# Optimization experiments

Measured on AMD Instinct MI355X. Metric: run time of the kernel, lower is better.

The kernel has to match this reference:

```python
import jax, jax.numpy as jnp
import numpy as np

SPATIAL = ((100, 100), (50, 50), (25, 25), (13, 13))
STARTS = [0]
for _h, _w in SPATIAL[:-1]:
    STARTS.append(STARTS[-1] + _h * _w)
L_TOTAL = sum(h * w for h, w in SPATIAL)  # 13294
D, DFFN, NL, NH, NP = 256, 1024, 4, 8, 4
DH = D // NH
EPS = 1e-5


def _ln(x, g, b):
    mu = x.mean(-1, keepdims=True)
    var = ((x - mu) ** 2).mean(-1, keepdims=True)
    return (x - mu) * jax.lax.rsqrt(var + EPS) * g + b


def _bilinear(v_l, x, y, H, W):
    # v_l: [B,NH,H*W,DH]; x,y: [B,NH,Q*NP] pixel coords (grid_sample align_corners=False, zero padding)
    x0f = jnp.floor(x); y0f = jnp.floor(y)
    lx, ly = x - x0f, y - y0f
    x0 = x0f.astype(jnp.int32); y0 = y0f.astype(jnp.int32)
    acc = 0.0
    for dx, dy, w in ((0, 0, (1 - lx) * (1 - ly)), (1, 0, lx * (1 - ly)),
                      (0, 1, (1 - lx) * ly), (1, 1, lx * ly)):
        xi, yi = x0 + dx, y0 + dy
        valid = (xi >= 0) & (xi < W) & (yi >= 0) & (yi < H)
        idx = jnp.clip(yi, 0, H - 1) * W + jnp.clip(xi, 0, W - 1)
        g = jnp.take_along_axis(v_l, idx[..., None], axis=2)  # [B,NH,Q*NP,DH]
        acc = acc + g * (w * valid.astype(w.dtype))[..., None]
    return acc


def _msdeform(query, value_in, ref, norm_wh, Woff, boff, Wattn, battn, Wval, bval, Wout, bout):
    B, Q, _ = query.shape
    v = (value_in @ Wval + bval).reshape(B, L_TOTAL, NH, DH)
    off = (query @ Woff + boff).reshape(B, Q, NH, NL, NP, 2)
    aw = (query @ Wattn + battn).reshape(B, Q, NH, NL * NP)
    aw = jax.nn.softmax(aw, axis=-1).reshape(B, Q, NH, NL, NP)
    # normalized sampling locations in [0,1]: ref + offset / (W,H)
    loc = ref[:, :, None, :, None, :] + off / norm_wh[None, None, None, :, None, :]
    out = 0.0
    for l, (H, W) in enumerate(SPATIAL):
        s = STARTS[l]
        v_l = v[:, s:s + H * W].transpose(0, 2, 1, 3)          # [B,NH,HW,DH]
        loc_l = loc[:, :, :, l].transpose(0, 2, 1, 3, 4)       # [B,NH,Q,NP,2]
        x = (loc_l[..., 0] * W - 0.5).reshape(B, NH, Q * NP)
        y = (loc_l[..., 1] * H - 0.5).reshape(B, NH, Q * NP)
        samp = _bilinear(v_l, x, y, H, W).reshape(B, NH, Q, NP, DH)
        w_l = aw[:, :, :, l].transpose(0, 2, 1, 3)             # [B,NH,Q,NP]
        out = out + (samp * w_l[..., None]).sum(3)             # [B,NH,Q,DH]
    out = out.transpose(0, 2, 1, 3).reshape(B, Q, D)
    return out @ Wout + bout


def setup_inputs() -> dict:
    key = jax.random.key(0)
    ks = jax.random.split(key, 12)
    B = 4
    s = 0.02
    return {
        "src": jax.random.normal(ks[0], (B, L_TOTAL, D), jnp.float32),
        "pos": jax.random.normal(ks[1], (B, L_TOTAL, D), jnp.float32),
        "reference_points": jax.random.uniform(ks[2], (B, L_TOTAL, NL, 2), jnp.float32),
        "spatial_shapes": jnp.array(SPATIAL, jnp.int32),
        "level_start_index": jnp.array(STARTS, jnp.int32),
        "W_off": jax.random.normal(ks[3], (D, NH * NL * NP * 2), jnp.float32) * 0.01,
        "b_off": jax.random.normal(ks[4], (NH * NL * NP * 2,), jnp.float32) * 0.5,
        "W_attn": jax.random.normal(ks[5], (D, NH * NL * NP), jnp.float32) * s,
        "b_attn": jnp.zeros((NH * NL * NP,), jnp.float32),
        "W_val": jax.random.normal(ks[6], (D, D), jnp.float32) * s,
        "b_val": jnp.zeros((D,), jnp.float32),
        "W_out": jax.random.normal(ks[7], (D, D), jnp.float32) * s,
        "b_out": jnp.zeros((D,), jnp.float32),
        "ln_sa_g": jnp.ones((D,), jnp.float32),
        "ln_sa_b": jnp.zeros((D,), jnp.float32),
        "W1": jax.random.normal(ks[8], (D, DFFN), jnp.float32) * s,
        "b1": jnp.zeros((DFFN,), jnp.float32),
        "W2": jax.random.normal(ks[9], (DFFN, D), jnp.float32) * s,
        "b2": jnp.zeros((D,), jnp.float32),
        "ln_ff_g": jnp.ones((D,), jnp.float32),
        "ln_ff_b": jnp.zeros((D,), jnp.float32),
    }


def reference(src, pos, reference_points, spatial_shapes, level_start_index,
              W_off, b_off, W_attn, b_attn, W_val, b_val, W_out, b_out,
              ln_sa_g, ln_sa_b, W1, b1, W2, b2, ln_ff_g, ln_ff_b):
    # offset normalizer is (W, H) per level
    norm_wh = jnp.stack([spatial_shapes[:, 1], spatial_shapes[:, 0]], -1).astype(src.dtype)
    q = src + pos  # with_pos_embed
    sa = _msdeform(q, src, reference_points, norm_wh,
                   W_off, b_off, W_attn, b_attn, W_val, b_val, W_out, b_out)
    x = _ln(sa + src, ln_sa_g, ln_sa_b)          # dropout = identity (eval)
    y = jnp.maximum(x @ W1 + b1, 0.0) @ W2 + b2  # relu FFN
    return _ln(y + x, ln_ff_g, ln_ff_b)
```

## Files before the change

### kernel.cpp

```cpp
#include <hip/hip_runtime.h>
#include <hip/hip_bf16.h>

typedef __hip_bfloat16 bf16;
typedef short bf16x8 __attribute__((ext_vector_type(8)));
typedef float f32x4  __attribute__((ext_vector_type(4)));

#define ROWS 53176
#define LTOT 13294

__device__ __forceinline__ float b2f(bf16 v) { return __bfloat162float(v); }

__device__ __forceinline__ void gl2lds16(const void* g, void* l) {
    __builtin_amdgcn_global_load_lds(
        (const __attribute__((address_space(1))) unsigned*)g,
        (__attribute__((address_space(3))) unsigned*)l, 16, 0, 0);
}

template<bool RELU>
__global__ __launch_bounds__(256)
void mfma_gemm_n(const bf16* __restrict__ A, const bf16* __restrict__ Bt,
                 const float* __restrict__ bias, bf16* __restrict__ C,
                 int M, int N, int K)
{
    __shared__ __align__(16) short As[128 * 32];
    __shared__ __align__(16) short Bs[128 * 32];
    const int tid  = threadIdx.x;
    const int wave = tid >> 6, lane = tid & 63;
    const int m0 = blockIdx.y * 128, n0 = blockIdx.x * 128;
    const int lrow = lane >> 2, lcol = lane & 3;
    const int quad = lane >> 4;

    f32x4 acc[4][4];
#pragma unroll
    for (int i = 0; i < 4; ++i)
#pragma unroll
        for (int j = 0; j < 4; ++j) acc[i][j] = (f32x4){0.f, 0.f, 0.f, 0.f};

    const int wM = (wave >> 1) * 64, wN = (wave & 1) * 64;
    const int foff = (lane & 15) * 32 + quad * 8;

    for (int kk = 0; kk < K; kk += 32) {
#pragma unroll
        for (int q = 0; q < 2; ++q) {
            int rbase = wave * 32 + q * 16;
            int row = rbase + lrow;
            gl2lds16(A  + (size_t)(m0 + row) * K + kk + lcol * 8, &As[rbase * 32]);
            gl2lds16(Bt + (size_t)(n0 + row) * K + kk + lcol * 8, &Bs[rbase * 32]);
        }
        __syncthreads();
        bf16x8 af[4], bfr[4];
#pragma unroll
        for (int i = 0; i < 4; ++i)
            af[i] = *(const bf16x8*)&As[(wM + i * 16) * 32 + foff];
#pragma unroll
        for (int j = 0; j < 4; ++j)
            bfr[j] = *(const bf16x8*)&Bs[(wN + j * 16) * 32 + foff];
#pragma unroll
        for (int i = 0; i < 4; ++i)
#pragma unroll
            for (int j = 0; j < 4; ++j)
                acc[i][j] = __builtin_amdgcn_mfma_f32_16x16x32_bf16(bfr[j], af[i], acc[i][j], 0, 0, 0);
        __syncthreads();
    }

    float4 b4[4];
#pragma unroll
    for (int j = 0; j < 4; ++j)
        b4[j] = *(const float4*)&bias[n0 + wN + j * 16 + quad * 4];

#pragma unroll
    for (int i = 0; i < 4; ++i) {
        int gm = m0 + wM + i * 16 + (lane & 15);
        if (gm >= M) continue;
#pragma unroll
        for (int j = 0; j < 4; ++j) {
            int gn = n0 + wN + j * 16 + quad * 4;
            union { bf16 h[4]; uint2 u2; } pk;
#pragma unroll
            for (int r = 0; r < 4; ++r) {
                float v = acc[i][j][r] + ((const float*)&b4[j])[r];
                if (RELU) v = fmaxf(v, 0.f);
                pk.h[r] = __float2bfloat16(v);
            }
            *(uint2*)&C[(size_t)gm * N + gn] = pk.u2;
        }
    }
}

template<typename OT>
__global__ __launch_bounds__(512)
void mfma_gemm_ln(const bf16* __restrict__ A, const bf16* __restrict__ Bt,
                  const float* __restrict__ bias, const bf16* __restrict__ res,
                  OT* __restrict__ C, const float* __restrict__ gam,
                  const float* __restrict__ bet, int M, int K)
{
    __shared__ __align__(16) short As[128 * 32];
    __shared__ __align__(16) short Bs[256 * 32];
    __shared__ float rsum[128], rsq[128];
    const int tid  = threadIdx.x;
    const int wave = tid >> 6, lane = tid & 63;
    const int m0 = blockIdx.x * 128;
    const int lrow = lane >> 2, lcol = lane & 3;
    const int quad = lane >> 4;
    if (tid < 128) { rsum[tid] = 0.f; rsq[tid] = 0.f; }

    f32x4 acc[4][4];
#pragma unroll
    for (int i = 0; i < 4; ++i)
#pragma unroll
        for (int j = 0; j < 4; ++j) acc[i][j] = (f32x4){0.f, 0.f, 0.f, 0.f};

    const int wM = (wave >> 2) * 64, wN = (wave & 3) * 64;
    const int foff = (lane & 15) * 32 + quad * 8;

    for (int kk = 0; kk < K; kk += 32) {
#pragma unroll
        for (int q = 0; q < 3; ++q) {
            int r = wave * 48 + q * 16;
            if (r < 128) {
                gl2lds16(A + (size_t)(m0 + r + lrow) * K + kk + lcol * 8, &As[r * 32]);
            } else {
                int rr = r - 128;
                gl2lds16(Bt + (size_t)(rr + lrow) * K + kk + lcol * 8, &Bs[rr * 32]);
            }
        }
        __syncthreads();
        bf16x8 af[4], bfr[4];
#pragma unroll
        for (int i = 0; i < 4; ++i)
            af[i] = *(const bf16x8*)&As[(wM + i * 16) * 32 + foff];
#pragma unroll
        for (int j = 0; j < 4; ++j)
            bfr[j] = *(const bf16x8*)&Bs[(wN + j * 16) * 32 + foff];
#pragma unroll
        for (int i = 0; i < 4; ++i)
#pragma unroll
            for (int j = 0; j < 4; ++j)
                acc[i][j] = __builtin_amdgcn_mfma_f32_16x16x32_bf16(bfr[j], af[i], acc[i][j], 0, 0, 0);
        __syncthreads();
    }

    float4 b4[4], g4[4], be4[4];
#pragma unroll
    for (int j = 0; j < 4; ++j) {
        int gn = wN + j * 16 + quad * 4;
        b4[j]  = *(const float4*)&bias[gn];
        g4[j]  = *(const float4*)&gam[gn];
        be4[j] = *(const float4*)&bet[gn];
    }

    float lsum[4], lsq[4];
#pragma unroll
    for (int i = 0; i < 4; ++i) {
        int gm = m0 + wM + i * 16 + (lane & 15);
        lsum[i] = 0.f; lsq[i] = 0.f;
#pragma unroll
        for (int j = 0; j < 4; ++j) {
            int gn = wN + j * 16 + quad * 4;
            float r4[4] = {0.f, 0.f, 0.f, 0.f};
            if (gm < M) {
                uint2 ru = *(const uint2*)&res[(size_t)gm * 256 + gn];
                const bf16* rh = (const bf16*)&ru;
#pragma unroll
                for (int r = 0; r < 4; ++r) r4[r] = b2f(rh[r]);
            }
#pragma unroll
            for (int r = 0; r < 4; ++r) {
                float v = acc[i][j][r] + ((const float*)&b4[j])[r] + r4[r];
                acc[i][j][r] = v;
                lsum[i] += v;
                lsq[i]  += v * v;
            }
        }
#pragma unroll
        for (int mask = 16; mask <= 32; mask <<= 1) {
            lsum[i] += __shfl_xor(lsum[i], mask);
            lsq[i]  += __shfl_xor(lsq[i], mask);
        }
    }
    if (quad == 0) {
#pragma unroll
        for (int i = 0; i < 4; ++i) {
            atomicAdd(&rsum[wM + i * 16 + (lane & 15)], lsum[i]);
            atomicAdd(&rsq [wM + i * 16 + (lane & 15)], lsq[i]);
        }
    }
    __syncthreads();

#pragma unroll
    for (int i = 0; i < 4; ++i) {
        int lr = wM + i * 16 + (lane & 15);
        int gm = m0 + lr;
        if (gm >= M) continue;
        float mean = rsum[lr] * (1.f / 256.f);
        float var  = rsq[lr] * (1.f / 256.f) - mean * mean;
        float rstd = rsqrtf(fmaxf(var, 0.f) + 1e-5f);
#pragma unroll
        for (int j = 0; j < 4; ++j) {
            int gn = wN + j * 16 + quad * 4;
            if constexpr (sizeof(OT) == 2) {
                union { bf16 h[4]; uint2 u2; } pk;
#pragma unroll
                for (int r = 0; r < 4; ++r)
                    pk.h[r] = __float2bfloat16((acc[i][j][r] - mean) * rstd *
                              ((const float*)&g4[j])[r] + ((const float*)&be4[j])[r]);
                *(uint2*)&((bf16*)C)[(size_t)gm * 256 + gn] = pk.u2;
            } else {
                float4 o;
#pragma unroll
                for (int r = 0; r < 4; ++r)
                    ((float*)&o)[r] = (acc[i][j][r] - mean) * rstd *
                              ((const float*)&g4[j])[r] + ((const float*)&be4[j])[r];
                *(float4*)&((float*)C)[(size_t)gm * 256 + gn] = o;
            }
        }
    }
}

__global__ void cast_qs_kernel(const float* __restrict__ s, const float* __restrict__ p,
                               bf16* __restrict__ sb, bf16* __restrict__ qb, int n4)
{
    int i = blockIdx.x * 256 + threadIdx.x;
    if (i >= n4) return;
    float4 sv = ((const float4*)s)[i];
    float4 pv = ((const float4*)p)[i];
    union { bf16 h[4]; uint2 u; } a, b;
    a.h[0] = __float2bfloat16(sv.x); a.h[1] = __float2bfloat16(sv.y);
    a.h[2] = __float2bfloat16(sv.z); a.h[3] = __float2bfloat16(sv.w);
    b.h[0] = __float2bfloat16(sv.x + pv.x); b.h[1] = __float2bfloat16(sv.y + pv.y);
    b.h[2] = __float2bfloat16(sv.z + pv.z); b.h[3] = __float2bfloat16(sv.w + pv.w);
    ((uint2*)sb)[i] = a.u;
    ((uint2*)qb)[i] = b.u;
}

__global__ void wcast_all(const float* __restrict__ Wval, const float* __restrict__ Woff,
                          const float* __restrict__ Wattn, const float* __restrict__ Wout,
                          const float* __restrict__ W1, const float* __restrict__ W2,
                          const float* __restrict__ boff, const float* __restrict__ battn,
                          bf16* __restrict__ Wval_t, bf16* __restrict__ Wcat_t,
                          bf16* __restrict__ Wout_t, bf16* __restrict__ W1_t,
                          bf16* __restrict__ W2_t, float* __restrict__ bcat)
{
    int e = blockIdx.x * 256 + threadIdx.x;
    if (e < 384) bcat[e] = (e < 256) ? boff[e] : battn[e - 256];
    if (e < 65536) {
        int n = e >> 8, k = e & 255;
        Wval_t[e] = __float2bfloat16(Wval[k * 256 + n]);
    } else if (e < 163840) {
        int i = e - 65536; int n = i >> 8, k = i & 255;
        float w = (n < 256) ? Woff[k * 256 + n] : Wattn[k * 128 + (n - 256)];
        Wcat_t[i] = __float2bfloat16(w);
    } else if (e < 229376) {
        int i = e - 163840; int n = i >> 8, k = i & 255;
        Wout_t[i] = __float2bfloat16(Wout[k * 256 + n]);
    } else if (e < 491520) {
        int i = e - 229376; int n = i >> 8, k = i & 255;
        W1_t[i] = __float2bfloat16(W1[k * 1024 + n]);
    } else if (e < 753664) {
        int i = e - 491520; int n = i >> 10, k = i & 1023;
        W2_t[i] = __float2bfloat16(W2[k * 256 + n]);
    }
}

__global__ __launch_bounds__(256)
void sample_kernel(const bf16* __restrict__ v, const bf16* __restrict__ ocat,
                   const float* __restrict__ ref, bf16* __restrict__ samp)
{
    __shared__ int4 tab[16][33];
    const int tid = threadIdx.x;
    const int grp = tid >> 4, lane = tid & 15;
    const int gidx = blockIdx.x * 16 + grp;
    const int h = gidx & 7, bq = gidx >> 3, b = bq / LTOT;

    {
        const int p = lane, l = p >> 2, pp = p & 3;
        const int W = (l == 0) ? 100 : (l == 1) ? 50 : (l == 2) ? 25 : 13;
        const int S = (l == 0) ? 0 : (l == 1) ? 10000 : (l == 2) ? 12500 : 13125;
        const float fW = (float)W;
        float rx = ref[(size_t)bq * 8 + l * 2 + 0];
        float ry = ref[(size_t)bq * 8 + l * 2 + 1];
        const bf16* ob = ocat + (size_t)bq * 384;
        float ox = b2f(ob[h * 32 + l * 8 + pp * 2 + 0]);
        float oy = b2f(ob[h * 32 + l * 8 + pp * 2 + 1]);
        float lg = b2f(ob[256 + h * 16 + p]);
        float m = lg;
#pragma unroll
        for (int mask = 1; mask <= 8; mask <<= 1) m = fmaxf(m, __shfl_xor(m, mask));
        float ev = __expf(lg - m);
        float s = ev;
#pragma unroll
        for (int mask = 1; mask <= 8; mask <<= 1) s += __shfl_xor(s, mask);
        float wgt = ev / s;

        float x = fmaf(rx, fW, ox - 0.5f);
        float y = fmaf(ry, fW, oy - 0.5f);
        float x0f = floorf(x), y0f = floorf(y);
        float lx = x - x0f, ly = y - y0f;
        int x0 = (int)x0f, y0 = (int)y0f;
        float tw[4] = {(1.f - lx) * (1.f - ly), lx * (1.f - ly),
                       (1.f - lx) * ly,         lx * ly};
        const int base = (b * LTOT + S) * 512 + h * 64;
        int  o[4]; float w[4];
#pragma unroll
        for (int t = 0; t < 4; ++t) {
            int xi = x0 + (t & 1), yi = y0 + (t >> 1);
            bool ok = (xi >= 0) & (xi < W) & (yi >= 0) & (yi < W);
            o[t] = ok ? base + (yi * W + xi) * 512 : 0;
            w[t] = ok ? wgt * tw[t] : 0.f;
        }
        tab[grp][p * 2 + 0] = make_int4(o[0], __float_as_int(w[0]), o[1], __float_as_int(w[1]));
        tab[grp][p * 2 + 1] = make_int4(o[2], __float_as_int(w[2]), o[3], __float_as_int(w[3]));
    }
    __syncthreads();

    const int lofs = lane * 4;
    const char* vc = (const char*)v;
    float a0 = 0.f, a1 = 0.f;
#pragma unroll 4
    for (int e2 = 0; e2 < 32; ++e2) {
        int4 q = tab[grp][e2];
        unsigned u0 = *(const unsigned*)(vc + (size_t)(unsigned)(q.x + lofs));
        unsigned u1 = *(const unsigned*)(vc + (size_t)(unsigned)(q.z + lofs));
        float w0 = __int_as_float(q.y), w1 = __int_as_float(q.w);
        a0 += w0 * __uint_as_float(u0 << 16);
        a1 += w0 * __uint_as_float(u0);
        a0 += w1 * __uint_as_float(u1 << 16);
        a1 += w1 * __uint_as_float(u1);
    }
    union { struct { bf16 a, b; } h2; unsigned u; } r;
    r.h2.a = __float2bfloat16(a0);
    r.h2.b = __float2bfloat16(a1);
    *(unsigned*)((char*)samp + (size_t)gidx * 64 + lane * 4) = r.u;
}

extern "C" void kernel_launch(void* const* d_in, const int* in_sizes, int n_in,
                              void* d_out, int out_size, void* d_ws, size_t ws_size,
                              hipStream_t stream)
{
    const float* src     = (const float*)d_in[0];
    const float* pos     = (const float*)d_in[1];
    const float* ref     = (const float*)d_in[2];
    const float* W_off   = (const float*)d_in[5];
    const float* b_off   = (const float*)d_in[6];
    const float* W_attn  = (const float*)d_in[7];
    const float* b_attn  = (const float*)d_in[8];
    const float* W_val   = (const float*)d_in[9];
    const float* b_val   = (const float*)d_in[10];
    const float* W_out   = (const float*)d_in[11];
    const float* b_out   = (const float*)d_in[12];
    const float* ln_sa_g = (const float*)d_in[13];
    const float* ln_sa_b = (const float*)d_in[14];
    const float* W1      = (const float*)d_in[15];
    const float* b1      = (const float*)d_in[16];
    const float* W2      = (const float*)d_in[17];
    const float* b2      = (const float*)d_in[18];
    const float* ln_ff_g = (const float*)d_in[19];
    const float* ln_ff_b = (const float*)d_in[20];

    char* ws = (char*)d_ws;
    bf16* sb     = (bf16*)(ws);
    bf16* qb     = (bf16*)(ws + 27226112);
    bf16* samp   = (bf16*)(ws + 27226112);
    bf16* vbuf   = (bf16*)(ws + 54452224);
    bf16* ocat   = (bf16*)(ws + 81678336);
    bf16* xb16   = (bf16*)(ws + 122517504);
    bf16* hbuf   = (bf16*)(ws);
    bf16* Wval_t = (bf16*)(ws + 149743616);
    bf16* Wcat_t = (bf16*)(ws + 149874688);
    float* bcat  = (float*)(ws + 150071296);
    bf16* Wout_t = (bf16*)(ws + 150072832);
    bf16* W1_t   = (bf16*)(ws + 150203904);
    bf16* W2_t   = (bf16*)(ws + 150728192);
    float* outf  = (float*)d_out;

    dim3 blk(256);

    cast_qs_kernel<<<dim3((ROWS * 64 + 255) / 256), blk, 0, stream>>>(src, pos, sb, qb, ROWS * 64);
    wcast_all<<<dim3(2944), blk, 0, stream>>>(W_val, W_off, W_attn, W_out, W1, W2,
                                              b_off, b_attn,
                                              Wval_t, Wcat_t, Wout_t, W1_t, W2_t, bcat);

    mfma_gemm_n<false><<<dim3(2, 416), blk, 0, stream>>>(sb, Wval_t, b_val, vbuf, ROWS, 256, 256);
    mfma_gemm_n<false><<<dim3(3, 416), blk, 0, stream>>>(qb, Wcat_t, bcat, ocat, ROWS, 384, 256);
    sample_kernel<<<dim3(ROWS * 8 / 16), blk, 0, stream>>>(vbuf, ocat, ref, samp);
    mfma_gemm_ln<bf16><<<dim3(416), dim3(512), 0, stream>>>(
        samp, Wout_t, b_out, sb, xb16, ln_sa_g, ln_sa_b, ROWS, 256);
    mfma_gemm_n<true><<<dim3(8, 416), blk, 0, stream>>>(xb16, W1_t, b1, hbuf, ROWS, 1024, 256);
    mfma_gemm_ln<float><<<dim3(416), dim3(512), 0, stream>>>(
        hbuf, W2_t, b2, xb16, outf, ln_ff_g, ln_ff_b, ROWS, 1024);
}
```

Measured before the change: 504.4 us.

## Keep weight tiles resident in swizzled LDS and stream activations from global

The GEMM kernels are restructured so the whole weight slice for a block's N-tile (full K) is loaded once into a 64KB XOR-swizzled LDS buffer. Each wave then reads its A rows directly from global memory, with no per-K-step LDS staging or barriers. The LayerNorm GEMMs now compute 32 rows per wave across all 256 columns and do the row reduction in-wave with shuffles, which removes the LDS atomics and the extra barrier. The trade-offs are higher register pressure (32 accumulators per lane), A loads from global that are not coalesced through LDS, and the large LDS footprint limiting occupancy to two blocks per CU.

New measurement: 541.6 us. 7.4% more time.

```diff
diff --git a/kernel.cpp b/kernel.cpp
--- a/kernel.cpp
+++ b/kernel.cpp
@@ -17,64 +17,72 @@
 }
 
 template<bool RELU>
-__global__ __launch_bounds__(256)
-void mfma_gemm_n(const bf16* __restrict__ A, const bf16* __restrict__ Bt,
-                 const float* __restrict__ bias, bf16* __restrict__ C,
-                 int M, int N, int K)
-{
-    __shared__ __align__(16) short As[128 * 32];
-    __shared__ __align__(16) short Bs[128 * 32];
+__global__ __launch_bounds__(256, 2)
+void gemm_bs_n(const bf16* __restrict__ A, const bf16* __restrict__ Bt,
+               const float* __restrict__ bias, bf16* __restrict__ C,
+               int M, int N)
+{
+    __shared__ __align__(16) char Bsb[65536];
     const int tid  = threadIdx.x;
     const int wave = tid >> 6, lane = tid & 63;
-    const int m0 = blockIdx.y * 128, n0 = blockIdx.x * 128;
-    const int lrow = lane >> 2, lcol = lane & 3;
-    const int quad = lane >> 4;
-
-    f32x4 acc[4][4];
+    const int l15 = lane & 15, quad = lane >> 4;
+    const int swz = (lane & 7) << 4;
+    const int m0 = blockIdx.y * 256, n0 = blockIdx.x * 128;
+
+    const char* Btb = (const char*)(Bt + (size_t)n0 * 256);
+#pragma unroll
+    for (int it = 0; it < 16; ++it) {
+        int c = it * 256 + tid;
+        int srcoff = (c * 16) ^ (((c >> 5) & 7) << 4);
+        gl2lds16(Btb + srcoff, Bsb + (it * 256 + wave * 64) * 16);
+    }
+
+    const bf16* aptr[4];
+#pragma unroll
+    for (int i = 0; i < 4; ++i) {
+        int r = m0 + wave * 64 + i * 16 + l15;
+        if (r > M - 1) r = M - 1;
+        aptr[i] = A + (size_t)r * 256;
+    }
+
+    f32x4 acc[4][8];
 #pragma unroll
     for (int i = 0; i < 4; ++i)
 #pragma unroll
-        for (int j = 0; j < 4; ++j) acc[i][j] = (f32x4){0.f, 0.f, 0.f, 0.f};
-
-    const int wM = (wave >> 1) * 64, wN = (wave & 1) * 64;
-    const int foff = (lane & 15) * 32 + quad * 8;
-
-    for (int kk = 0; kk < K; kk += 32) {
-#pragma unroll
-        for (int q = 0; q < 2; ++q) {
-            int rbase = wave * 32 + q * 16;
-            int row = rbase + lrow;
-            gl2lds16(A  + (size_t)(m0 + row) * K + kk + lcol * 8, &As[rbase * 32]);
-            gl2lds16(Bt + (size_t)(n0 + row) * K + kk + lcol * 8, &Bs[rbase * 32]);
-        }
-        __syncthreads();
-        bf16x8 af[4], bfr[4];
+        for (int j = 0; j < 8; ++j) acc[i][j] = (f32x4){0.f, 0.f, 0.f, 0.f};
+
+    __syncthreads();
+
+#pragma unroll
+    for (int kc = 0; kc < 8; ++kc) {
+        bf16x8 af[4], bfr[8];
 #pragma unroll
         for (int i = 0; i < 4; ++i)
-            af[i] = *(const bf16x8*)&As[(wM + i * 16) * 32 + foff];
-#pragma unroll
-        for (int j = 0; j < 4; ++j)
-            bfr[j] = *(const bf16x8*)&Bs[(wN + j * 16) * 32 + foff];
+            af[i] = *(const bf16x8*)(aptr[i] + kc * 32 + quad * 8);
+#pragma unroll
+        for (int j = 0; j < 8; ++j) {
+            int boff = ((j * 16 + l15) * 512 + kc * 64 + quad * 16) ^ swz;
+            bfr[j] = *(const bf16x8*)&Bsb[boff];
+        }
 #pragma unroll
         for (int i = 0; i < 4; ++i)
 #pragma unroll
-            for (int j = 0; j < 4; ++j)
+            for (int j = 0; j < 8; ++j)
                 acc[i][j] = __builtin_amdgcn_mfma_f32_16x16x32_bf16(bfr[j], af[i], acc[i][j], 0, 0, 0);
-        __syncthreads();
-    }
-
-    float4 b4[4];
-#pragma unroll
-    for (int j = 0; j < 4; ++j)
-        b4[j] = *(const float4*)&bias[n0 + wN + j * 16 + quad * 4];
+    }
+
+    float4 b4[8];
+#pragma unroll
+    for (int j = 0; j < 8; ++j)
+        b4[j] = *(const float4*)&bias[n0 + j * 16 + quad * 4];
 
 #pragma unroll
     for (int i = 0; i < 4; ++i) {
-        int gm = m0 + wM + i * 16 + (lane & 15);
+        int gm = m0 + wave * 64 + i * 16 + l15;
         if (gm >= M) continue;
 #pragma unroll
-        for (int j = 0; j < 4; ++j) {
-            int gn = n0 + wN + j * 16 + quad * 4;
+        for (int j = 0; j < 8; ++j) {
+            int gn = n0 + j * 16 + quad * 4;
             union { bf16 h[4]; uint2 u2; } pk;
 #pragma unroll
             for (int r = 0; r < 4; ++r) {
@@ -87,78 +95,75 @@
     }
 }
 
-template<typename OT>
-__global__ __launch_bounds__(512)
-void mfma_gemm_ln(const bf16* __restrict__ A, const bf16* __restrict__ Bt,
-                  const float* __restrict__ bias, const bf16* __restrict__ res,
-                  OT* __restrict__ C, const float* __restrict__ gam,
-                  const float* __restrict__ bet, int M, int K)
-{
-    __shared__ __align__(16) short As[128 * 32];
-    __shared__ __align__(16) short Bs[256 * 32];
-    __shared__ float rsum[128], rsq[128];
+template<typename OT, int K>
+__global__ __launch_bounds__(256, 2)
+void gemm_bs_ln(const bf16* __restrict__ A, const bf16* __restrict__ Bt,
+                const float* __restrict__ bias, const bf16* __restrict__ res,
+                OT* __restrict__ C, const float* __restrict__ gam,
+                const float* __restrict__ bet, int M)
+{
+    __shared__ __align__(16) char Bsb[65536];
     const int tid  = threadIdx.x;
     const int wave = tid >> 6, lane = tid & 63;
+    const int l15 = lane & 15, quad = lane >> 4;
+    const int swz = (lane & 7) << 4;
     const int m0 = blockIdx.x * 128;
-    const int lrow = lane >> 2, lcol = lane & 3;
-    const int quad = lane >> 4;
-    if (tid < 128) { rsum[tid] = 0.f; rsq[tid] = 0.f; }
-
-    f32x4 acc[4][4];
-#pragma unroll
-    for (int i = 0; i < 4; ++i)
-#pragma unroll
-        for (int j = 0; j < 4; ++j) acc[i][j] = (f32x4){0.f, 0.f, 0.f, 0.f};
-
-    const int wM = (wave >> 2) * 64, wN = (wave & 3) * 64;
-    const int foff = (lane & 15) * 32 + quad * 8;
-
-    for (int kk = 0; kk < K; kk += 32) {
-#pragma unroll
-        for (int q = 0; q < 3; ++q) {
-            int r = wave * 48 + q * 16;
-            if (r < 128) {
-                gl2lds16(A + (size_t)(m0 + r + lrow) * K + kk + lcol * 8, &As[r * 32]);
-            } else {
-                int rr = r - 128;
-                gl2lds16(Bt + (size_t)(rr + lrow) * K + kk + lcol * 8, &Bs[rr * 32]);
-            }
+
+    const bf16* aptr[2];
+#pragma unroll
+    for (int i = 0; i < 2; ++i) {
+        int r = m0 + wave * 32 + i * 16 + l15;
+        if (r > M - 1) r = M - 1;
+        aptr[i] = A + (size_t)r * K;
+    }
+
+    f32x4 acc[2][16];
+#pragma unroll
+    for (int i = 0; i < 2; ++i)
+#pragma unroll
+        for (int j = 0; j < 16; ++j) acc[i][j] = (f32x4){0.f, 0.f, 0.f, 0.f};
+
+    for (int kc = 0; kc < K / 128; ++kc) {
+#pragma unroll
+        for (int it = 0; it < 16; ++it) {
+            int c = it * 256 + tid;
+            int row = c >> 4, col = c & 15;
+            size_t srcoff = (size_t)row * (K * 2) + kc * 256
+                          + ((col * 16) ^ ((row & 7) << 4));
+            gl2lds16((const char*)Bt + srcoff, Bsb + (it * 256 + wave * 64) * 16);
         }
         __syncthreads();
-        bf16x8 af[4], bfr[4];
-#pragma unroll
-        for (int i = 0; i < 4; ++i)
-            af[i] = *(const bf16x8*)&As[(wM + i * 16) * 32 + foff];
-#pragma unroll
-        for (int j = 0; j < 4; ++j)
-            bfr[j] = *(const bf16x8*)&Bs[(wN + j * 16) * 32 + foff];
-#pragma unroll
-        for (int i = 0; i < 4; ++i)
-#pragma unroll
-            for (int j = 0; j < 4; ++j)
-                acc[i][j] = __builtin_amdgcn_mfma_f32_16x16x32_bf16(bfr[j], af[i], acc[i][j], 0, 0, 0);
+#pragma unroll
+        for (int t = 0; t < 4; ++t) {
+            bf16x8 af[2], bfr[16];
+#pragma unroll
+            for (int i = 0; i < 2; ++i)
+                af[i] = *(const bf16x8*)(aptr[i] + kc * 128 + t * 32 + quad * 8);
+#pragma unroll
+            for (int j = 0; j < 16; ++j) {
+                int boff = ((j * 16 + l15) * 256 + t * 64 + quad * 16) ^ swz;
+                bfr[j] = *(const bf16x8*)&Bsb[boff];
+            }
+#pragma unroll
+            for (int i = 0; i < 2; ++i)
+#pragma unroll
+                for (int j = 0; j < 16; ++j)
+                    acc[i][j] = __builtin_amdgcn_mfma_f32_16x16x32_bf16(bfr[j], af[i], acc[i][j], 0, 0, 0);
+        }
         __syncthreads();
     }
 
-    float4 b4[4], g4[4], be4[4];
-#pragma unroll
-    for (int j = 0; j < 4; ++j) {
-        int gn = wN + j * 16 + quad * 4;
-        b4[j]  = *(const float4*)&bias[gn];
-        g4[j]  = *(const float4*)&gam[gn];
-        be4[j] = *(const float4*)&bet[gn];
-    }
-
-    float lsum[4], lsq[4];
-#pragma unroll
-    for (int i = 0; i < 4; ++i) {
-        int gm = m0 + wM + i * 16 + (lane & 15);
-        lsum[i] = 0.f; lsq[i] = 0.f;
-#pragma unroll
-        for (int j = 0; j < 4; ++j) {
-            int gn = wN + j * 16 + quad * 4;
+#pragma unroll
+    for (int i = 0; i < 2; ++i) {
+        int gm = m0 + wave * 32 + i * 16 + l15;
+        bool valid = gm < M;
+        float lsum = 0.f, lsq = 0.f;
+#pragma unroll
+        for (int j = 0; j < 16; ++j) {
+            int gn = j * 16 + quad * 4;
+            float4 b4 = *(const float4*)&bias[gn];
             float r4[4] = {0.f, 0.f, 0.f, 0.f};
-            if (gm < M) {
+            if (valid) {
                 uint2 ru = *(const uint2*)&res[(size_t)gm * 256 + gn];
                 const bf16* rh = (const bf16*)&ru;
 #pragma unroll
@@ -166,51 +171,39 @@
             }
 #pragma unroll
             for (int r = 0; r < 4; ++r) {
-                float v = acc[i][j][r] + ((const float*)&b4[j])[r] + r4[r];
+                float v = acc[i][j][r] + ((const float*)&b4)[r] + r4[r];
                 acc[i][j][r] = v;
-                lsum[i] += v;
-                lsq[i]  += v * v;
+                lsum += v;
+                lsq  += v * v;
             }
         }
 #pragma unroll
         for (int mask = 16; mask <= 32; mask <<= 1) {
-            lsum[i] += __shfl_xor(lsum[i], mask);
-            lsq[i]  += __shfl_xor(lsq[i], mask);
-        }
-    }
-    if (quad == 0) {
-#pragma unroll
-        for (int i = 0; i < 4; ++i) {
-            atomicAdd(&rsum[wM + i * 16 + (lane & 15)], lsum[i]);
-            atomicAdd(&rsq [wM + i * 16 + (lane & 15)], lsq[i]);
-        }
-    }
-    __syncthreads();
-
-#pragma unroll
-    for (int i = 0; i < 4; ++i) {
-        int lr = wM + i * 16 + (lane & 15);
-        int gm = m0 + lr;
-        if (gm >= M) continue;
-        float mean = rsum[lr] * (1.f / 256.f);
-        float var  = rsq[lr] * (1.f / 256.f) - mean * mean;
+            lsum += __shfl_xor(lsum, mask);
+            lsq  += __shfl_xor(lsq, mask);
+        }
+        if (!valid) continue;
+        float mean = lsum * (1.f / 256.f);
+        float var  = lsq * (1.f / 256.f) - mean * mean;
         float rstd = rsqrtf(fmaxf(var, 0.f) + 1e-5f);
 #pragma unroll
-        for (int j = 0; j < 4; ++j) {
-            int gn = wN + j * 16 + quad * 4;
+        for (int j = 0; j < 16; ++j) {
+            int gn = j * 16 + quad * 4;
+            float4 g4  = *(const float4*)&gam[gn];
+            float4 be4 = *(const float4*)&bet[gn];
             if constexpr (sizeof(OT) == 2) {
                 union { bf16 h[4]; uint2 u2; } pk;
 #pragma unroll
                 for (int r = 0; r < 4; ++r)
                     pk.h[r] = __float2bfloat16((acc[i][j][r] - mean) * rstd *
-                              ((const float*)&g4[j])[r] + ((const float*)&be4[j])[r]);
+                              ((const float*)&g4)[r] + ((const float*)&be4)[r]);
                 *(uint2*)&((bf16*)C)[(size_t)gm * 256 + gn] = pk.u2;
             } else {
                 float4 o;
 #pragma unroll
                 for (int r = 0; r < 4; ++r)
                     ((float*)&o)[r] = (acc[i][j][r] - mean) * rstd *
-                              ((const float*)&g4[j])[r] + ((const float*)&be4[j])[r];
+                              ((const float*)&g4)[r] + ((const float*)&be4)[r];
                 *(float4*)&((float*)C)[(size_t)gm * 256 + gn] = o;
             }
         }
@@ -380,12 +373,12 @@
                                               b_off, b_attn,
                                               Wval_t, Wcat_t, Wout_t, W1_t, W2_t, bcat);
 
-    mfma_gemm_n<false><<<dim3(2, 416), blk, 0, stream>>>(sb, Wval_t, b_val, vbuf, ROWS, 256, 256);
-    mfma_gemm_n<false><<<dim3(3, 416), blk, 0, stream>>>(qb, Wcat_t, bcat, ocat, ROWS, 384, 256);
+    gemm_bs_n<false><<<dim3(2, 208), blk, 0, stream>>>(sb, Wval_t, b_val, vbuf, ROWS, 256);
+    gemm_bs_n<false><<<dim3(3, 208), blk, 0, stream>>>(qb, Wcat_t, bcat, ocat, ROWS, 384);
     sample_kernel<<<dim3(ROWS * 8 / 16), blk, 0, stream>>>(vbuf, ocat, ref, samp);
-    mfma_gemm_ln<bf16><<<dim3(416), dim3(512), 0, stream>>>(
-        samp, Wout_t, b_out, sb, xb16, ln_sa_g, ln_sa_b, ROWS, 256);
-    mfma_gemm_n<true><<<dim3(8, 416), blk, 0, stream>>>(xb16, W1_t, b1, hbuf, ROWS, 1024, 256);
-    mfma_gemm_ln<float><<<dim3(416), dim3(512), 0, stream>>>(
-        hbuf, W2_t, b2, xb16, outf, ln_ff_g, ln_ff_b, ROWS, 1024);
-}
+    gemm_bs_ln<bf16, 256><<<dim3(416), blk, 0, stream>>>(
+        samp, Wout_t, b_out, sb, xb16, ln_sa_g, ln_sa_b, ROWS);
+    gemm_bs_n<true><<<dim3(8, 208), blk, 0, stream>>>(xb16, W1_t, b1, hbuf, ROWS, 1024);
+    gemm_bs_ln<float, 1024><<<dim3(416), blk, 0, stream>>>(
+        hbuf, W2_t, b2, xb16, outf, ln_ff_g, ln_ff_b, ROWS);
+}
```

## Double-buffer LDS in MFMA GEMMs, swizzle LDS layout, remap workgroups across XCDs

Applied to the files above, without the earlier changes.

Both GEMM kernels now use two LDS buffers, so the async global-to-LDS load of the next K tile overlaps MFMA compute on the current one, with one barrier per iteration instead of two. The 16-byte chunks within each LDS row are XOR-swizzled by row to reduce bank conflicts on the fragment reads. The plain GEMM also remaps workgroup IDs in groups of eight, presumably to improve L2 locality across XCDs. LDS use doubles, which may lower occupancy, and the overlap relies on the async load completing in time before the barrier.

New measurement: 475.1 us. -5.8%, faster.

```diff
diff --git a/kernel.cpp b/kernel.cpp
--- a/kernel.cpp
+++ b/kernel.cpp
@@ -22,13 +22,19 @@
                  const float* __restrict__ bias, bf16* __restrict__ C,
                  int M, int N, int K)
 {
-    __shared__ __align__(16) short As[128 * 32];
-    __shared__ __align__(16) short Bs[128 * 32];
+    __shared__ __align__(16) short As[2][128 * 32];
+    __shared__ __align__(16) short Bs[2][128 * 32];
     const int tid  = threadIdx.x;
     const int wave = tid >> 6, lane = tid & 63;
-    const int m0 = blockIdx.y * 128, n0 = blockIdx.x * 128;
+
+    const int nwg  = gridDim.x * gridDim.y;
+    const int orig = blockIdx.y * gridDim.x + blockIdx.x;
+    const int wgid = ((nwg & 7) == 0) ? ((orig & 7) * (nwg >> 3) + (orig >> 3)) : orig;
+    const int bx = wgid % gridDim.x, by = wgid / gridDim.x;
+
+    const int m0 = by * 128, n0 = bx * 128;
     const int lrow = lane >> 2, lcol = lane & 3;
-    const int quad = lane >> 4;
+    const int quad = lane >> 4, l15 = lane & 15;
 
     f32x4 acc[4][4];
 #pragma unroll
@@ -37,31 +43,49 @@
         for (int j = 0; j < 4; ++j) acc[i][j] = (f32x4){0.f, 0.f, 0.f, 0.f};
 
     const int wM = (wave >> 1) * 64, wN = (wave & 1) * 64;
-    const int foff = (lane & 15) * 32 + quad * 8;
-
-    for (int kk = 0; kk < K; kk += 32) {
+
+    auto stage = [&](int p, int kk) {
 #pragma unroll
         for (int q = 0; q < 2; ++q) {
             int rbase = wave * 32 + q * 16;
             int row = rbase + lrow;
-            gl2lds16(A  + (size_t)(m0 + row) * K + kk + lcol * 8, &As[rbase * 32]);
-            gl2lds16(Bt + (size_t)(n0 + row) * K + kk + lcol * 8, &Bs[rbase * 32]);
-        }
-        __syncthreads();
+            int sw = (lcol * 16) ^ ((row & 3) << 4);
+            gl2lds16((const char*)(A  + (size_t)(m0 + row) * K + kk) + sw, &As[p][rbase * 32]);
+            gl2lds16((const char*)(Bt + (size_t)(n0 + row) * K + kk) + sw, &Bs[p][rbase * 32]);
+        }
+    };
+
+    auto compute = [&](int p) {
         bf16x8 af[4], bfr[4];
 #pragma unroll
-        for (int i = 0; i < 4; ++i)
-            af[i] = *(const bf16x8*)&As[(wM + i * 16) * 32 + foff];
-#pragma unroll
-        for (int j = 0; j < 4; ++j)
-            bfr[j] = *(const bf16x8*)&Bs[(wN + j * 16) * 32 + foff];
+        for (int i = 0; i < 4; ++i) {
+            int row = wM + i * 16 + l15;
+            af[i] = *(const bf16x8*)((const char*)&As[p][row * 32]
+                                     + ((quad * 16) ^ ((row & 3) << 4)));
+        }
+#pragma unroll
+        for (int j = 0; j < 4; ++j) {
+            int row = wN + j * 16 + l15;
+            bfr[j] = *(const bf16x8*)((const char*)&Bs[p][row * 32]
+                                      + ((quad * 16) ^ ((row & 3) << 4)));
+        }
 #pragma unroll
         for (int i = 0; i < 4; ++i)
 #pragma unroll
             for (int j = 0; j < 4; ++j)
                 acc[i][j] = __builtin_amdgcn_mfma_f32_16x16x32_bf16(bfr[j], af[i], acc[i][j], 0, 0, 0);
+    };
+
+    stage(0, 0);
+    __syncthreads();
+    int p = 0;
+    for (int kk = 32; kk < K; kk += 32) {
+        stage(p ^ 1, kk);
+        compute(p);
         __syncthreads();
-    }
+        p ^= 1;
+    }
+    compute(p);
 
     float4 b4[4];
 #pragma unroll
@@ -70,7 +94,7 @@
 
 #pragma unroll
     for (int i = 0; i < 4; ++i) {
-        int gm = m0 + wM + i * 16 + (lane & 15);
+        int gm = m0 + wM + i * 16 + l15;
         if (gm >= M) continue;
 #pragma unroll
         for (int j = 0; j < 4; ++j) {
@@ -94,14 +118,14 @@
                   OT* __restrict__ C, const float* __restrict__ gam,
                   const float* __restrict__ bet, int M, int K)
 {
-    __shared__ __align__(16) short As[128 * 32];
-    __shared__ __align__(16) short Bs[256 * 32];
+    __shared__ __align__(16) short As[2][128 * 32];
+    __shared__ __align__(16) short Bs[2][256 * 32];
     __shared__ float rsum[128], rsq[128];
     const int tid  = threadIdx.x;
     const int wave = tid >> 6, lane = tid & 63;
     const int m0 = blockIdx.x * 128;
     const int lrow = lane >> 2, lcol = lane & 3;
-    const int quad = lane >> 4;
+    const int quad = lane >> 4, l15 = lane & 15;
     if (tid < 128) { rsum[tid] = 0.f; rsq[tid] = 0.f; }
 
     f32x4 acc[4][4];
@@ -111,34 +135,56 @@
         for (int j = 0; j < 4; ++j) acc[i][j] = (f32x4){0.f, 0.f, 0.f, 0.f};
 
     const int wM = (wave >> 2) * 64, wN = (wave & 3) * 64;
-    const int foff = (lane & 15) * 32 + quad * 8;
-
-    for (int kk = 0; kk < K; kk += 32) {
+
+    auto stage = [&](int p, int kk) {
 #pragma unroll
         for (int q = 0; q < 3; ++q) {
             int r = wave * 48 + q * 16;
+            int sw;
             if (r < 128) {
-                gl2lds16(A + (size_t)(m0 + r + lrow) * K + kk + lcol * 8, &As[r * 32]);
+                int row = r + lrow;
+                sw = (lcol * 16) ^ ((row & 3) << 4);
+                gl2lds16((const char*)(A + (size_t)(m0 + row) * K + kk) + sw, &As[p][r * 32]);
             } else {
                 int rr = r - 128;
-                gl2lds16(Bt + (size_t)(rr + lrow) * K + kk + lcol * 8, &Bs[rr * 32]);
+                int row = rr + lrow;
+                sw = (lcol * 16) ^ ((row & 3) << 4);
+                gl2lds16((const char*)(Bt + (size_t)(row) * K + kk) + sw, &Bs[p][rr * 32]);
             }
         }
-        __syncthreads();
+    };
+
+    auto compute = [&](int p) {
         bf16x8 af[4], bfr[4];
 #pragma unroll
-        for (int i = 0; i < 4; ++i)
-            af[i] = *(const bf16x8*)&As[(wM + i * 16) * 32 + foff];
-#pragma unroll
-        for (int j = 0; j < 4; ++j)
-            bfr[j] = *(const bf16x8*)&Bs[(wN + j * 16) * 32 + foff];
+        for (int i = 0; i < 4; ++i) {
+            int row = wM + i * 16 + l15;
+            af[i] = *(const bf16x8*)((const char*)&As[p][row * 32]
+                                     + ((quad * 16) ^ ((row & 3) << 4)));
+        }
+#pragma unroll
+        for (int j = 0; j < 4; ++j) {
+            int row = wN + j * 16 + l15;
+            bfr[j] = *(const bf16x8*)((const char*)&Bs[p][row * 32]
+                                      + ((quad * 16) ^ ((row & 3) << 4)));
+        }
 #pragma unroll
         for (int i = 0; i < 4; ++i)
 #pragma unroll
             for (int j = 0; j < 4; ++j)
                 acc[i][j] = __builtin_amdgcn_mfma_f32_16x16x32_bf16(bfr[j], af[i], acc[i][j], 0, 0, 0);
+    };
+
+    stage(0, 0);
+    __syncthreads();
+    int p = 0;
+    for (int kk = 32; kk < K; kk += 32) {
+        stage(p ^ 1, kk);
+        compute(p);
         __syncthreads();
-    }
+        p ^= 1;
+    }
+    compute(p);
 
     float4 b4[4], g4[4], be4[4];
 #pragma unroll
@@ -152,7 +198,7 @@
     float lsum[4], lsq[4];
 #pragma unroll
     for (int i = 0; i < 4; ++i) {
-        int gm = m0 + wM + i * 16 + (lane & 15);
+        int gm = m0 + wM + i * 16 + l15;
         lsum[i] = 0.f; lsq[i] = 0.f;
 #pragma unroll
         for (int j = 0; j < 4; ++j) {
@@ -181,15 +227,15 @@
     if (quad == 0) {
 #pragma unroll
         for (int i = 0; i < 4; ++i) {
-            atomicAdd(&rsum[wM + i * 16 + (lane & 15)], lsum[i]);
-            atomicAdd(&rsq [wM + i * 16 + (lane & 15)], lsq[i]);
+            atomicAdd(&rsum[wM + i * 16 + l15], lsum[i]);
+            atomicAdd(&rsq [wM + i * 16 + l15], lsq[i]);
         }
     }
     __syncthreads();
 
 #pragma unroll
     for (int i = 0; i < 4; ++i) {
-        int lr = wM + i * 16 + (lane & 15);
+        int lr = wM + i * 16 + l15;
         int gm = m0 + lr;
         if (gm >= M) continue;
         float mean = rsum[lr] * (1.f / 256.f);
```
